# Optimization experiments

Hardware: AMD Instinct MI355X
Metric: run time of the kernel (lower is better)

## Reference

```python
import jax, jax.numpy as jnp
import numpy as np

B, N, DIM, HEADS, DEPTH, MLP = 4, 1024, 256, 4, 4, 1024
DH = DIM // HEADS
EPS = 1e-5


def _ln(x, g, b):
    mu = jnp.mean(x, axis=-1, keepdims=True)
    var = jnp.mean((x - mu) ** 2, axis=-1, keepdims=True)
    return (x - mu) / jnp.sqrt(var + EPS) * g + b


def setup_inputs() -> dict:
    key = jax.random.key(0)
    ks = jax.random.split(key, 10)
    s = 0.02
    p = {}
    p["x"] = jax.random.normal(ks[0], (B, N, DIM), jnp.float32)
    p["attn_bias"] = jax.random.normal(ks[1], (2, B, HEADS, N, N), jnp.float32)
    p["ln1_g"] = jnp.ones((DEPTH, DIM), jnp.float32)
    p["ln1_b"] = jnp.zeros((DEPTH, DIM), jnp.float32)
    p["Wkv"] = jax.random.normal(ks[2], (DEPTH, DIM, 2 * DIM), jnp.float32) * s
    p["Wq"] = jax.random.normal(ks[3], (DEPTH, DIM, DIM), jnp.float32) * s
    p["Wo"] = jax.random.normal(ks[4], (DEPTH, DIM, DIM), jnp.float32) * s
    p["bo"] = jnp.zeros((DEPTH, DIM), jnp.float32)
    p["ln2_g"] = jnp.ones((DEPTH, DIM), jnp.float32)
    p["ln2_b"] = jnp.zeros((DEPTH, DIM), jnp.float32)
    p["W1"] = jax.random.normal(ks[5], (DEPTH, DIM, MLP), jnp.float32) * s
    p["b1"] = jnp.zeros((DEPTH, MLP), jnp.float32)
    p["W2"] = jax.random.normal(ks[6], (DEPTH, MLP, DIM), jnp.float32) * s
    p["b2"] = jnp.zeros((DEPTH, DIM), jnp.float32)
    p["Wg"] = jax.random.normal(ks[7], (DIM, DIM), jnp.float32) * s
    p["lng_g"] = jnp.ones((DIM,), jnp.float32)
    p["lng_b"] = jnp.zeros((DIM,), jnp.float32)
    return p


def reference(x, attn_bias, ln1_g, ln1_b, Wkv, Wq, Wo, bo, ln2_g, ln2_b, W1, b1, W2, b2, Wg, lng_g, lng_b):
    scale = DIM ** -0.5
    add_attn = attn_bias[0] + attn_bias[1]            # [B,H,N,N]
    # aggregation bias matrices are layer-invariant (recomputed identically each layer in torch)
    A = jnp.mean(attn_bias[0], axis=1)                # [B,N,N]
    S = jnp.mean(attn_bias[1], axis=1)
    G = jax.nn.softmax(A * S, axis=2)                 # [B,N,N]

    def split_heads(t):  # [B,N,DIM] -> [B,H,N,DH]
        return t.reshape(B, N, HEADS, DH).transpose(0, 2, 1, 3)

    for l in range(DEPTH):
        # softmax-GCN aggregation
        x_ma = jax.nn.relu(_ln(jnp.matmul(G, x) @ Wg, lng_g, lng_b))
        # attention (PreNorm on x only; q comes from un-normed x_ma)
        xn = _ln(x, ln1_g[l], ln1_b[l])
        kv = xn @ Wkv[l]
        k, v = jnp.split(kv, 2, axis=-1)
        q = x_ma @ Wq[l]
        qh, kh, vh = split_heads(q), split_heads(k), split_heads(v)
        dots = jnp.einsum('bhid,bhjd->bhij', qh, kh) * scale + add_attn
        attn = jax.nn.softmax(dots, axis=-1)
        out = jnp.einsum('bhij,bhjd->bhid', attn, vh)
        out = out.transpose(0, 2, 1, 3).reshape(B, N, DIM)
        x = x + out @ Wo[l] + bo[l]
        # feed-forward (exact GELU, matching torch nn.GELU default)
        xn2 = _ln(x, ln2_g[l], ln2_b[l])
        x = x + jax.nn.gelu(xn2 @ W1[l] + b1[l], approximate=False) @ W2[l] + b2[l]
    return x
```

## Files before the change

### kernel.cpp

```cpp
#include <hip/hip_runtime.h>
#include <hip/hip_bf16.h>
#include <math.h>

typedef unsigned short u16;
typedef __bf16 bf16x8 __attribute__((ext_vector_type(8)));
typedef float f32x4 __attribute__((ext_vector_type(4)));

#define B_ 4
#define N_ 1024
#define DIM_ 256
#define HEADS_ 4
#define DH_ 64
#define MLP_ 1024
#define DEPTH_ 4

__device__ __forceinline__ float r2f(u16 r){ return __uint_as_float(((unsigned)r)<<16); }
__device__ __forceinline__ u16 f2r(float f){ __hip_bfloat16 h = __float2bfloat16(f); return *(u16*)&h; }

__device__ __forceinline__ float gelu_exact(float v){
  return 0.5f*v*(1.0f + erff(v*0.70710678118654752440f));
}

#define MFMA16(a,b,c) __builtin_amdgcn_mfma_f32_16x16x32_bf16(a,b,c,0,0,0)

__global__ void prep_fused(const float* __restrict__ bias, u16* __restrict__ G, u16* __restrict__ bsum,
                           const float* __restrict__ X, u16* __restrict__ Y,
                           const float* __restrict__ g, const float* __restrict__ bvec){
  if (blockIdx.x < 4096){
    int blk = blockIdx.x;
    int i = blk & (N_-1);
    int b = blk >> 10;
    int t = threadIdx.x;
    __shared__ float red[256];
    long long base0 = ((long long)(b*HEADS_)*N_ + i)*(long long)N_;
    const long long hs = (long long)N_*N_;
    const long long cs = (long long)B_*HEADS_*N_*N_;
    int j0 = t*4;
    f32x4 a = {0.f,0.f,0.f,0.f}, s = {0.f,0.f,0.f,0.f};
    #pragma unroll
    for (int h=0;h<HEADS_;h++){
      f32x4 x0 = *(const f32x4*)(bias + base0 + h*hs + j0);
      f32x4 x1 = *(const f32x4*)(bias + cs + base0 + h*hs + j0);
      a += x0; s += x1;
      union { ushort4 u; u16 e[4]; } pk;
      #pragma unroll
      for (int k=0;k<4;k++) pk.e[k] = f2r(x0[k]+x1[k]);
      *(ushort4*)(bsum + base0 + h*hs + j0) = pk.u;
    }
    float v[4]; float lmax = -3e38f;
    #pragma unroll
    for (int k=0;k<4;k++){ v[k] = (a[k]*0.25f)*(s[k]*0.25f); lmax = fmaxf(lmax, v[k]); }
    red[t]=lmax; __syncthreads();
    for (int st=128;st>0;st>>=1){ if(t<st) red[t]=fmaxf(red[t],red[t+st]); __syncthreads(); }
    float m = red[0]; __syncthreads();
    float e[4]; float lsum = 0.f;
    #pragma unroll
    for (int k=0;k<4;k++){ e[k] = __expf(v[k]-m); lsum += e[k]; }
    red[t]=lsum; __syncthreads();
    for (int st=128;st>0;st>>=1){ if(t<st) red[t]+=red[t+st]; __syncthreads(); }
    float inv = 1.0f/red[0];
    u16* Grow = G + ((long long)b*N_ + i)*(long long)N_;
    union { ushort4 u; u16 e[4]; } pg;
    #pragma unroll
    for (int k=0;k<4;k++) pg.e[k] = f2r(e[k]*inv);
    *(ushort4*)(Grow + j0) = pg.u;
  } else {
    int row = (blockIdx.x-4096)*8 + (threadIdx.x>>5);
    int cg = threadIdx.x&31;
    const float* xp = X + (long long)row*DIM_ + cg*8;
    f32x4 v0 = *(const f32x4*)xp;
    f32x4 v1 = *(const f32x4*)(xp+4);
    float s = v0[0]+v0[1]+v0[2]+v0[3]+v1[0]+v1[1]+v1[2]+v1[3];
    s += __shfl_xor(s,1); s += __shfl_xor(s,2); s += __shfl_xor(s,4); s += __shfl_xor(s,8); s += __shfl_xor(s,16);
    float mu = s*(1.0f/256.0f);
    float s2 = 0.f;
    #pragma unroll
    for (int k=0;k<4;k++){ float d=v0[k]-mu; s2 += d*d; }
    #pragma unroll
    for (int k=0;k<4;k++){ float d=v1[k]-mu; s2 += d*d; }
    s2 += __shfl_xor(s2,1); s2 += __shfl_xor(s2,2); s2 += __shfl_xor(s2,4); s2 += __shfl_xor(s2,8); s2 += __shfl_xor(s2,16);
    float rstd = rsqrtf(s2*(1.0f/256.0f)+1e-5f);
    f32x4 g0 = *(const f32x4*)(g + cg*8);
    f32x4 g1 = *(const f32x4*)(g + cg*8 + 4);
    f32x4 b0 = *(const f32x4*)(bvec + cg*8);
    f32x4 b1 = *(const f32x4*)(bvec + cg*8 + 4);
    union { ushort4 u[2]; u16 e[8]; } pk;
    #pragma unroll
    for (int k=0;k<4;k++) pk.e[k]   = f2r((v0[k]-mu)*rstd*g0[k] + b0[k]);
    #pragma unroll
    for (int k=0;k<4;k++) pk.e[4+k] = f2r((v1[k]-mu)*rstd*g1[k] + b1[k]);
    u16* yp = Y + (long long)row*DIM_ + cg*8;
    *(ushort4*)yp = pk.u[0];
    *(ushort4*)(yp+4) = pk.u[1];
  }
}

__global__ void tcast_all(const float* __restrict__ Wkv, const float* __restrict__ Wq,
                          const float* __restrict__ Wo, const float* __restrict__ W1,
                          const float* __restrict__ W2, const float* __restrict__ Wg,
                          const float* __restrict__ xin,
                          u16* WkvT, u16* WqT, u16* WoT, u16* W1T, u16* W2T, u16* WgT, u16* xT){
  int z = blockIdx.z;
  const float* I; u16* O; int ldin, R, C;
  if (z < 4)       { I = Wkv + z*131072;      O = WkvT + z*131072;      ldin=512;  R=256;  C=512;  }
  else if (z < 8)  { I = Wq  + (z-4)*65536;   O = WqT  + (z-4)*65536;   ldin=256;  R=256;  C=256;  }
  else if (z < 12) { I = Wo  + (z-8)*65536;   O = WoT  + (z-8)*65536;   ldin=256;  R=256;  C=256;  }
  else if (z < 16) { I = W1  + (z-12)*262144; O = W1T  + (z-12)*262144; ldin=1024; R=256;  C=1024; }
  else if (z < 20) { I = W2  + (z-16)*262144; O = W2T  + (z-16)*262144; ldin=256;  R=1024; C=256;  }
  else if (z == 20){ I = Wg;                  O = WgT;                  ldin=256;  R=256;  C=256;  }
  else             { I = xin + (z-21)*262144; O = xT   + (z-21)*262144; ldin=256;  R=1024; C=256;  }
  int c0 = blockIdx.x*32, r0 = blockIdx.y*32;
  if (c0 >= C || r0 >= R) return;
  __shared__ float tile[32][33];
  int tx = threadIdx.x, ty = threadIdx.y;
  #pragma unroll
  for (int i=0;i<4;i++)
    tile[ty*4+i][tx] = I[(long long)(r0+ty*4+i)*ldin + c0+tx];
  __syncthreads();
  #pragma unroll
  for (int i=0;i<4;i++)
    O[(long long)(c0+ty*4+i)*R + r0+tx] = f2r(tile[tx][ty*4+i]);
}

__global__ __launch_bounds__(512, 4) void layer_pre(
    const u16* __restrict__ Gb, const u16* __restrict__ xT, const u16* __restrict__ xnb,
    const u16* __restrict__ WgT, const u16* __restrict__ WqT, const u16* __restrict__ WkvT,
    const float* __restrict__ lng, const float* __restrict__ lnb,
    u16* __restrict__ qb, u16* __restrict__ kvb, u16* __restrict__ vt)
{
  __shared__ float Gx_s[16][264];
  __shared__ float t2_s[16][264];
  __shared__ u16  xma_s[16][264];
  int tid = threadIdx.x;
  int w = tid>>6, lane = tid&63, lr = lane&15, qd = lane>>4;
  int bid = blockIdx.x;

  if (bid >= 256){
    int row0 = (bid-256)*16;
    int batch = row0>>10;
    const u16* Ap = xnb + (long long)(row0+lr)*DIM_;
    f32x4 acc[4] = {};
    for (int k0=0;k0<256;k0+=32){
      bf16x8 af = *(const bf16x8*)(Ap + k0 + qd*8);
      #pragma unroll
      for (int i=0;i<4;i++){
        bf16x8 bf = *(const bf16x8*)(WkvT + (long long)((w*4+i)*16+lr)*256 + k0 + qd*8);
        acc[i] = MFMA16(af,bf,acc[i]);
      }
    }
    #pragma unroll
    for (int i=0;i<4;i++){
      int col = (w*4+i)*16+lr;
      #pragma unroll
      for (int r=0;r<4;r++){
        int row = row0+qd*4+r;
        float v = acc[i][r];
        kvb[(long long)row*512 + col] = f2r(v);
        if (col >= 256)
          vt[(long long)batch*262144 + (long long)(col-256)*1024 + (row&1023)] = f2r(v);
      }
    }
    return;
  }

  int row0 = bid*16;
  int batch = row0>>10, brow0 = row0&1023;

  {
    int kw = w>>2, cw = w&3;
    const u16* Ap = Gb + (long long)batch*1048576 + (long long)(brow0+lr)*1024 + kw*512;
    const u16* Bp = xT + (long long)batch*262144 + (long long)kw*512;
    f32x4 acc[4] = {};
    for (int k0=0;k0<512;k0+=32){
      bf16x8 af = *(const bf16x8*)(Ap + k0 + qd*8);
      #pragma unroll
      for (int nt=0;nt<4;nt++){
        bf16x8 bf = *(const bf16x8*)(Bp + (long long)(cw*64+nt*16+lr)*1024 + k0 + qd*8);
        acc[nt] = MFMA16(af,bf,acc[nt]);
      }
    }
    if (kw==0){
      #pragma unroll
      for (int nt=0;nt<4;nt++)
        #pragma unroll
        for (int r=0;r<4;r++) Gx_s[qd*4+r][cw*64+nt*16+lr] = acc[nt][r];
    }
    __syncthreads();
    if (kw==1){
      #pragma unroll
      for (int nt=0;nt<4;nt++)
        #pragma unroll
        for (int r=0;r<4;r++) Gx_s[qd*4+r][cw*64+nt*16+lr] += acc[nt][r];
    }
    __syncthreads();
  }
  {
    int r = tid>>5, cg2 = tid&31;
    #pragma unroll
    for (int i=0;i<8;i++) xma_s[r][cg2*8+i] = f2r(Gx_s[r][cg2*8+i]);
  }
  __syncthreads();
  {
    f32x4 acc[2] = {};
    for (int k0=0;k0<256;k0+=32){
      bf16x8 af = *(const bf16x8*)&xma_s[lr][k0+qd*8];
      #pragma unroll
      for (int i=0;i<2;i++){
        bf16x8 bf = *(const bf16x8*)(WgT + (long long)((w*2+i)*16+lr)*256 + k0 + qd*8);
        acc[i] = MFMA16(af,bf,acc[i]);
      }
    }
    #pragma unroll
    for (int i=0;i<2;i++)
      #pragma unroll
      for (int r=0;r<4;r++) t2_s[qd*4+r][(w*2+i)*16+lr] = acc[i][r];
  }
  __syncthreads();
  {
    int r = tid>>5, cg2 = tid&31;
    float v[8]; float s=0.f;
    #pragma unroll
    for (int i=0;i<8;i++){ v[i] = t2_s[r][cg2*8+i]; s += v[i]; }
    s += __shfl_xor(s,1); s += __shfl_xor(s,2); s += __shfl_xor(s,4); s += __shfl_xor(s,8); s += __shfl_xor(s,16);
    float mu = s*(1.0f/256.0f);
    float s2=0.f;
    #pragma unroll
    for (int i=0;i<8;i++){ float d=v[i]-mu; s2 += d*d; }
    s2 += __shfl_xor(s2,1); s2 += __shfl_xor(s2,2); s2 += __shfl_xor(s2,4); s2 += __shfl_xor(s2,8); s2 += __shfl_xor(s2,16);
    float rstd = rsqrtf(s2*(1.0f/256.0f)+1e-5f);
    #pragma unroll
    for (int i=0;i<8;i++){
      int c = cg2*8+i;
      float y = (v[i]-mu)*rstd*lng[c] + lnb[c];
      xma_s[r][c] = f2r(fmaxf(y,0.f));
    }
  }
  __syncthreads();
  {
    f32x4 acc[2] = {};
    for (int k0=0;k0<256;k0+=32){
      bf16x8 af = *(const bf16x8*)&xma_s[lr][k0+qd*8];
      #pragma unroll
      for (int i=0;i<2;i++){
        bf16x8 bf = *(const bf16x8*)(WqT + (long long)((w*2+i)*16+lr)*256 + k0 + qd*8);
        acc[i] = MFMA16(af,bf,acc[i]);
      }
    }
    #pragma unroll
    for (int i=0;i<2;i++)
      #pragma unroll
      for (int r=0;r<4;r++)
        qb[(long long)(row0+qd*4+r)*DIM_ + (w*2+i)*16+lr] = f2r(acc[i][r]);
  }
}

#define APSMEM 84224
__global__ __launch_bounds__(1024, 4) void attn_post(
    const u16* __restrict__ qb, const u16* __restrict__ kvb,
    const u16* __restrict__ vt, const u16* __restrict__ bsum,
    const float* __restrict__ resx,
    const u16* __restrict__ WoT, const float* __restrict__ bo,
    const float* __restrict__ ln2g, const float* __restrict__ ln2b,
    const u16* __restrict__ W1T, const float* __restrict__ b1,
    const u16* __restrict__ W2T, const float* __restrict__ b2,
    float* __restrict__ xf_out,
    const float* __restrict__ ln1g_next, const float* __restrict__ ln1b_next,
    u16* __restrict__ xn_out, u16* __restrict__ xT_out)
{
  __shared__ __align__(16) char smem[APSMEM];
  u16 (*sb)[16][72]   = (u16 (*)[16][72])smem;
  u16 (*Pl)[16][72]   = (u16 (*)[16][72])(smem+36864);
  float (*Ml)[16]     = (float(*)[16])(smem+73728);
  float (*Ll)[16]     = (float(*)[16])(smem+74752);
  float (*Ol)[16][68] = (float(*)[16][68])smem;
  u16  (*ao_s)[264]   = (u16 (*)[264])(smem+75776);
  float (*v_s)[264]   = (float(*)[264])smem;
  u16  (*xn2_s)[264]  = (u16 (*)[264])(smem+16896);
  u16  (*h1_s)[1048]  = (u16 (*)[1048])(smem+25344);
  float (*xnew_s)[264]= (float(*)[264])(smem+58880);

  int tid = threadIdx.x;
  int w = tid>>6, lane = tid&63, lr = lane&15, qd = lane>>4;
  int row0 = blockIdx.x*16;
  int batch = row0>>10, brow0 = row0&1023;

  f32x4 oacc[4] = {};
  float m_r[4] = {-3e38f,-3e38f,-3e38f,-3e38f};
  float l_r[4] = {0.f,0.f,0.f,0.f};
  {
    int h = w>>2, g = w&3;
    int z = batch*HEADS_ + h;
    const u16* qp = qb + ((long long)row0 + lr)*DIM_ + h*DH_;
    bf16x8 aq0 = *(const bf16x8*)(qp + qd*8);
    bf16x8 aq1 = *(const bf16x8*)(qp + 32 + qd*8);

    const u16* kbase = kvb + ((long long)(batch*N_))*512 + h*DH_;
    const u16* vbase = vt + (long long)batch*(DIM_*N_) + (long long)(h*DH_)*N_;
    const u16* bias_base = bsum + ((long long)z*N_ + brow0)*(long long)N_;
    int srr = lane>>2, scc = (lane&3)*16;

    for (int jtl=0; jtl<4; jtl++){
      int j0 = (g*4 + jtl)*64;
      {
        const u16* gs = bias_base + (long long)srr*N_ + j0 + scc;
        uint4 t0 = *(const uint4*)gs;
        uint4 t1 = *(const uint4*)(gs+8);
        *(uint4*)&sb[w][srr][scc]   = t0;
        *(uint4*)&sb[w][srr][scc+8] = t1;
      }
      f32x4 sacc[4] = {};
      #pragma unroll
      for (int nt=0; nt<4; nt++){
        const u16* kp = kbase + (long long)(j0 + nt*16 + lr)*512;
        bf16x8 bk0 = *(const bf16x8*)(kp + qd*8);
        bf16x8 bk1 = *(const bf16x8*)(kp + 32 + qd*8);
        sacc[nt] = MFMA16(aq0, bk0, sacc[nt]);
        sacc[nt] = MFMA16(aq1, bk1, sacc[nt]);
      }
      #pragma unroll
      for (int r=0;r<4;r++){
        float pv[4];
        float vmax = -3e38f;
        #pragma unroll
        for (int nt=0;nt<4;nt++){
          float v = sacc[nt][r]*0.0625f + r2f(sb[w][qd*4+r][nt*16+lr]);
          pv[nt] = v;
          vmax = fmaxf(vmax, v);
        }
        vmax = fmaxf(vmax, __shfl_xor(vmax,1));
        vmax = fmaxf(vmax, __shfl_xor(vmax,2));
        vmax = fmaxf(vmax, __shfl_xor(vmax,4));
        vmax = fmaxf(vmax, __shfl_xor(vmax,8));
        float newm = fmaxf(m_r[r], vmax);
        float alpha = __expf(m_r[r]-newm);
        m_r[r] = newm;
        float psum = 0.f;
        #pragma unroll
        for (int nt=0;nt<4;nt++){
          float p = __expf(pv[nt]-newm);
          psum += p;
          Pl[w][qd*4+r][nt*16+lr] = f2r(p);
        }
        psum += __shfl_xor(psum,1);
        psum += __shfl_xor(psum,2);
        psum += __shfl_xor(psum,4);
        psum += __shfl_xor(psum,8);
        l_r[r] = l_r[r]*alpha + psum;
        #pragma unroll
        for (int ot=0;ot<4;ot++) oacc[ot][r] *= alpha;
      }
      #pragma unroll
      for (int ks=0;ks<2;ks++){
        bf16x8 ap = *(const bf16x8*)&Pl[w][lr][ks*32 + qd*8];
        #pragma unroll
        for (int ot=0;ot<4;ot++){
          const u16* vp = vbase + (long long)(ot*16+lr)*N_ + j0 + ks*32 + qd*8;
          bf16x8 bv = *(const bf16x8*)vp;
          oacc[ot] = MFMA16(ap, bv, oacc[ot]);
        }
      }
    }
  }
  __syncthreads();
  #pragma unroll
  for (int r=0;r<4;r++){
    int row = qd*4+r;
    #pragma unroll
    for (int ot=0;ot<4;ot++) Ol[w][row][ot*16+lr] = oacc[ot][r];
    if (lr==0){ Ml[w][row] = m_r[r]; Ll[w][row] = l_r[r]; }
  }
  __syncthreads();
  if ((w&3)==0){
    int h = w>>2;
    #pragma unroll
    for (int r=0;r<4;r++){
      int row = qd*4+r;
      float m0 = Ml[w][row], m1 = Ml[w+1][row], m2 = Ml[w+2][row], m3 = Ml[w+3][row];
      float mm = fmaxf(fmaxf(m0,m1), fmaxf(m2,m3));
      float e0 = __expf(m0-mm), e1 = __expf(m1-mm), e2 = __expf(m2-mm), e3 = __expf(m3-mm);
      float inv = 1.0f/(Ll[w][row]*e0 + Ll[w+1][row]*e1 + Ll[w+2][row]*e2 + Ll[w+3][row]*e3);
      #pragma unroll
      for (int ot=0;ot<4;ot++){
        int c = ot*16+lr;
        float o = Ol[w][row][c]*e0 + Ol[w+1][row][c]*e1 + Ol[w+2][row][c]*e2 + Ol[w+3][row][c]*e3;
        ao_s[row][h*DH_ + c] = f2r(o*inv);
      }
    }
  }
  __syncthreads();

  {
    int kw = w>>3, cw = w&7;
    f32x4 acc[2] = {};
    for (int k0=0;k0<128;k0+=32){
      bf16x8 af = *(const bf16x8*)&ao_s[lr][kw*128 + k0 + qd*8];
      #pragma unroll
      for (int i=0;i<2;i++){
        int cv = cw*2+i;
        bf16x8 bf = *(const bf16x8*)(WoT + (long long)(cv*16+lr)*256 + kw*128 + k0 + qd*8);
        acc[i] = MFMA16(af,bf,acc[i]);
      }
    }
    if (kw==0){
      #pragma unroll
      for (int i=0;i<2;i++)
        #pragma unroll
        for (int r=0;r<4;r++) v_s[qd*4+r][(cw*2+i)*16+lr] = acc[i][r];
    }
    __syncthreads();
    if (kw==1){
      #pragma unroll
      for (int i=0;i<2;i++){
        int col = (cw*2+i)*16+lr;
        #pragma unroll
        for (int r=0;r<4;r++)
          v_s[qd*4+r][col] = v_s[qd*4+r][col] + acc[i][r] + bo[col]
                           + resx[(long long)(row0+qd*4+r)*DIM_ + col];
      }
    }
    __syncthreads();
  }
  {
    int r = tid>>6, c0 = (tid&63)*4;
    float v[4]; float s=0.f;
    #pragma unroll
    for (int i=0;i<4;i++){ v[i] = v_s[r][c0+i]; s += v[i]; }
    s += __shfl_xor(s,1); s += __shfl_xor(s,2); s += __shfl_xor(s,4);
    s += __shfl_xor(s,8); s += __shfl_xor(s,16); s += __shfl_xor(s,32);
    float mu = s*(1.0f/256.0f);
    float s2=0.f;
    #pragma unroll
    for (int i=0;i<4;i++){ float d=v[i]-mu; s2 += d*d; }
    s2 += __shfl_xor(s2,1); s2 += __shfl_xor(s2,2); s2 += __shfl_xor(s2,4);
    s2 += __shfl_xor(s2,8); s2 += __shfl_xor(s2,16); s2 += __shfl_xor(s2,32);
    float rstd = rsqrtf(s2*(1.0f/256.0f)+1e-5f);
    #pragma unroll
    for (int i=0;i<4;i++){
      int c = c0+i;
      xn2_s[r][c] = f2r((v[i]-mu)*rstd*ln2g[c] + ln2b[c]);
    }
  }
  __syncthreads();
  {
    f32x4 acc[4] = {};
    for (int k0=0;k0<256;k0+=32){
      bf16x8 af = *(const bf16x8*)&xn2_s[lr][k0+qd*8];
      #pragma unroll
      for (int i=0;i<4;i++){
        int cv = w*4+i;
        bf16x8 bf = *(const bf16x8*)(W1T + (long long)(cv*16+lr)*256 + k0 + qd*8);
        acc[i] = MFMA16(af,bf,acc[i]);
      }
    }
    #pragma unroll
    for (int i=0;i<4;i++){
      int col = (w*4+i)*16+lr;
      #pragma unroll
      for (int r=0;r<4;r++)
        h1_s[qd*4+r][col] = f2r(gelu_exact(acc[i][r] + b1[col]));
    }
  }
  __syncthreads();
  {
    int kw = w>>3, cw = w&7;
    f32x4 acc[2] = {};
    for (int k0=0;k0<512;k0+=32){
      bf16x8 af = *(const bf16x8*)&h1_s[lr][kw*512 + k0 + qd*8];
      #pragma unroll
      for (int i=0;i<2;i++){
        int cv = cw*2+i;
        bf16x8 bf = *(const bf16x8*)(W2T + (long long)(cv*16+lr)*1024 + kw*512 + k0 + qd*8);
        acc[i] = MFMA16(af,bf,acc[i]);
      }
    }
    if (kw==0){
      #pragma unroll
      for (int i=0;i<2;i++)
        #pragma unroll
        for (int r=0;r<4;r++) xnew_s[qd*4+r][(cw*2+i)*16+lr] = acc[i][r];
    }
    __syncthreads();
    if (kw==1){
      #pragma unroll
      for (int i=0;i<2;i++){
        int col = (cw*2+i)*16+lr;
        #pragma unroll
        for (int r=0;r<4;r++){
          float v = xnew_s[qd*4+r][col] + acc[i][r] + b2[col] + v_s[qd*4+r][col];
          xf_out[(long long)(row0+qd*4+r)*DIM_ + col] = v;
          xnew_s[qd*4+r][col] = v;
        }
      }
    }
  }
  if (ln1g_next){
    __syncthreads();
    int r = tid>>6, c0 = (tid&63)*4;
    float v[4]; float s=0.f;
    #pragma unroll
    for (int i=0;i<4;i++){ v[i] = xnew_s[r][c0+i]; s += v[i]; }
    s += __shfl_xor(s,1); s += __shfl_xor(s,2); s += __shfl_xor(s,4);
    s += __shfl_xor(s,8); s += __shfl_xor(s,16); s += __shfl_xor(s,32);
    float mu = s*(1.0f/256.0f);
    float s2=0.f;
    #pragma unroll
    for (int i=0;i<4;i++){ float d=v[i]-mu; s2 += d*d; }
    s2 += __shfl_xor(s2,1); s2 += __shfl_xor(s2,2); s2 += __shfl_xor(s2,4);
    s2 += __shfl_xor(s2,8); s2 += __shfl_xor(s2,16); s2 += __shfl_xor(s2,32);
    float rstd = rsqrtf(s2*(1.0f/256.0f)+1e-5f);
    int grow = row0 + r;
    #pragma unroll
    for (int i=0;i<4;i++){
      int c = c0+i;
      xn_out[(long long)grow*DIM_ + c] = f2r((v[i]-mu)*rstd*ln1g_next[c] + ln1b_next[c]);
      xT_out[(long long)batch*262144 + (long long)c*1024 + (grow&1023)] = f2r(v[i]);
    }
  }
}

extern "C" void kernel_launch(void* const* d_in, const int* in_sizes, int n_in,
                              void* d_out, int out_size, void* d_ws, size_t ws_size,
                              hipStream_t stream){
  const float* x_in   = (const float*)d_in[0];
  const float* abias  = (const float*)d_in[1];
  const float* ln1_g  = (const float*)d_in[2];
  const float* ln1_b  = (const float*)d_in[3];
  const float* Wkv    = (const float*)d_in[4];
  const float* Wq     = (const float*)d_in[5];
  const float* Wo     = (const float*)d_in[6];
  const float* bo     = (const float*)d_in[7];
  const float* ln2_g  = (const float*)d_in[8];
  const float* ln2_b  = (const float*)d_in[9];
  const float* W1     = (const float*)d_in[10];
  const float* b1     = (const float*)d_in[11];
  const float* W2     = (const float*)d_in[12];
  const float* b2     = (const float*)d_in[13];
  const float* Wg     = (const float*)d_in[14];
  const float* lng_g  = (const float*)d_in[15];
  const float* lng_b  = (const float*)d_in[16];

  char* ws = (char*)d_ws;
  float* xf   = (float*)(ws);
  u16*  Gb    = (u16*)(ws + (4ll<<20));
  u16*  bsum  = (u16*)(ws + (12ll<<20));
  u16*  kvb   = (u16*)(ws + (44ll<<20));
  u16*  vt    = (u16*)(ws + (48ll<<20));
  u16*  xT    = (u16*)(ws + (50ll<<20));
  u16*  xnb   = (u16*)(ws + (52ll<<20));
  u16*  qb    = (u16*)(ws + (54ll<<20));
  u16*  WkvT  = (u16*)(ws + (58ll<<20));
  u16*  WqT   = (u16*)(ws + (59ll<<20));
  u16*  WoT   = (u16*)(ws + (59ll<<20) + (512ll<<10));
  u16*  W1T   = (u16*)(ws + (60ll<<20));
  u16*  W2T   = (u16*)(ws + (62ll<<20));
  u16*  WgT   = (u16*)(ws + (64ll<<20));

  prep_fused<<<dim3(4608), dim3(256), 0, stream>>>(abias, Gb, bsum, x_in, xnb, ln1_g, ln1_b);
  tcast_all<<<dim3(32,32,25), dim3(32,8), 0, stream>>>(Wkv,Wq,Wo,W1,W2,Wg,x_in,
                                                       WkvT,WqT,WoT,W1T,W2T,WgT,xT);

  for (int l=0; l<DEPTH_; l++){
    const float* resx = (l==0) ? x_in : xf;
    layer_pre<<<dim3(512), dim3(512), 0, stream>>>(Gb, xT, xnb,
        WgT, WqT + (long long)l*65536, WkvT + (long long)l*131072,
        lng_g, lng_b, qb, kvb, vt);
    if (l < DEPTH_-1){
      attn_post<<<dim3(256), dim3(1024), 0, stream>>>(qb, kvb, vt, bsum, resx,
          WoT + (long long)l*65536, bo + l*DIM_, ln2_g + l*DIM_, ln2_b + l*DIM_,
          W1T + (long long)l*262144, b1 + l*MLP_, W2T + (long long)l*262144, b2 + l*DIM_,
          xf, ln1_g + (l+1)*DIM_, ln1_b + (l+1)*DIM_, xnb, xT);
    } else {
      attn_post<<<dim3(256), dim3(1024), 0, stream>>>(qb, kvb, vt, bsum, resx,
          WoT + (long long)l*65536, bo + l*DIM_, ln2_g + l*DIM_, ln2_b + l*DIM_,
          W1T + (long long)l*262144, b1 + l*MLP_, W2T + (long long)l*262144, b2 + l*DIM_,
          (float*)d_out, nullptr, nullptr, nullptr, nullptr);
    }
  }
}
```

Before: 702.5 us.

## Shrink attn_post LDS via pairwise softmax merge and buffer aliasing

Reuses the bias staging buffer for the P tile, merges the four per-head partial softmax states in a two-step pairwise tree instead of all at once, and aliases the FFN output scratch onto existing buffers. This cuts the kernel's shared memory from about 84 KB to about 59 KB and raises the launch-bounds occupancy hint so more blocks can fit per CU. In exchange it adds extra barriers. The tighter register budget from the higher occupancy hint may also cause spills.

```diff
diff --git a/kernel.cpp b/kernel.cpp
--- a/kernel.cpp
+++ b/kernel.cpp
@@ -254,8 +254,8 @@
   }
 }
 
-#define APSMEM 84224
-__global__ __launch_bounds__(1024, 4) void attn_post(
+#define APSMEM 58880
+__global__ __launch_bounds__(1024, 8) void attn_post(
     const u16* __restrict__ qb, const u16* __restrict__ kvb,
     const u16* __restrict__ vt, const u16* __restrict__ bsum,
     const float* __restrict__ resx,
@@ -269,26 +269,25 @@
 {
   __shared__ __align__(16) char smem[APSMEM];
   u16 (*sb)[16][72]   = (u16 (*)[16][72])smem;
-  u16 (*Pl)[16][72]   = (u16 (*)[16][72])(smem+36864);
-  float (*Ml)[16]     = (float(*)[16])(smem+73728);
-  float (*Ll)[16]     = (float(*)[16])(smem+74752);
-  float (*Ol)[16][68] = (float(*)[16][68])smem;
-  u16  (*ao_s)[264]   = (u16 (*)[264])(smem+75776);
+  float (*Olb)[16][68]= (float(*)[16][68])smem;
+  float (*Mlb)[16]    = (float(*)[16])(smem+34816);
+  float (*Llb)[16]    = (float(*)[16])(smem+35328);
+  u16  (*ao_s)[264]   = (u16 (*)[264])(smem+36864);
   float (*v_s)[264]   = (float(*)[264])smem;
   u16  (*xn2_s)[264]  = (u16 (*)[264])(smem+16896);
   u16  (*h1_s)[1048]  = (u16 (*)[1048])(smem+25344);
-  float (*xnew_s)[264]= (float(*)[264])(smem+58880);
+  float (*p3_s)[264]  = (float(*)[264])(smem+25344);
 
   int tid = threadIdx.x;
   int w = tid>>6, lane = tid&63, lr = lane&15, qd = lane>>4;
   int row0 = blockIdx.x*16;
   int batch = row0>>10, brow0 = row0&1023;
+  int h = w>>2, g = w&3;
 
   f32x4 oacc[4] = {};
   float m_r[4] = {-3e38f,-3e38f,-3e38f,-3e38f};
   float l_r[4] = {0.f,0.f,0.f,0.f};
   {
-    int h = w>>2, g = w&3;
     int z = batch*HEADS_ + h;
     const u16* qp = qb + ((long long)row0 + lr)*DIM_ + h*DH_;
     bf16x8 aq0 = *(const bf16x8*)(qp + qd*8);
@@ -339,7 +338,7 @@
         for (int nt=0;nt<4;nt++){
           float p = __expf(pv[nt]-newm);
           psum += p;
-          Pl[w][qd*4+r][nt*16+lr] = f2r(p);
+          sb[w][qd*4+r][nt*16+lr] = f2r(p);
         }
         psum += __shfl_xor(psum,1);
         psum += __shfl_xor(psum,2);
@@ -351,7 +350,7 @@
       }
       #pragma unroll
       for (int ks=0;ks<2;ks++){
-        bf16x8 ap = *(const bf16x8*)&Pl[w][lr][ks*32 + qd*8];
+        bf16x8 ap = *(const bf16x8*)&sb[w][lr][ks*32 + qd*8];
         #pragma unroll
         for (int ot=0;ot<4;ot++){
           const u16* vp = vbase + (long long)(ot*16+lr)*N_ + j0 + ks*32 + qd*8;
@@ -362,28 +361,55 @@
     }
   }
   __syncthreads();
-  #pragma unroll
-  for (int r=0;r<4;r++){
-    int row = qd*4+r;
-    #pragma unroll
-    for (int ot=0;ot<4;ot++) Ol[w][row][ot*16+lr] = oacc[ot][r];
-    if (lr==0){ Ml[w][row] = m_r[r]; Ll[w][row] = l_r[r]; }
-  }
-  __syncthreads();
-  if ((w&3)==0){
-    int h = w>>2;
+  if (g & 1){
+    int slot = h*2 + (g>>1);
     #pragma unroll
     for (int r=0;r<4;r++){
       int row = qd*4+r;
-      float m0 = Ml[w][row], m1 = Ml[w+1][row], m2 = Ml[w+2][row], m3 = Ml[w+3][row];
-      float mm = fmaxf(fmaxf(m0,m1), fmaxf(m2,m3));
-      float e0 = __expf(m0-mm), e1 = __expf(m1-mm), e2 = __expf(m2-mm), e3 = __expf(m3-mm);
-      float inv = 1.0f/(Ll[w][row]*e0 + Ll[w+1][row]*e1 + Ll[w+2][row]*e2 + Ll[w+3][row]*e3);
+      #pragma unroll
+      for (int ot=0;ot<4;ot++) Olb[slot][row][ot*16+lr] = oacc[ot][r];
+      if (lr==0){ Mlb[slot][row] = m_r[r]; Llb[slot][row] = l_r[r]; }
+    }
+  }
+  __syncthreads();
+  if (!(g & 1)){
+    int slot = h*2 + (g>>1);
+    #pragma unroll
+    for (int r=0;r<4;r++){
+      int row = qd*4+r;
+      float m1 = Mlb[slot][row], l1 = Llb[slot][row];
+      float mm = fmaxf(m_r[r], m1);
+      float e0 = __expf(m_r[r]-mm), e1 = __expf(m1-mm);
+      m_r[r] = mm;
+      l_r[r] = l_r[r]*e0 + l1*e1;
+      #pragma unroll
+      for (int ot=0;ot<4;ot++)
+        oacc[ot][r] = oacc[ot][r]*e0 + Olb[slot][row][ot*16+lr]*e1;
+    }
+  }
+  __syncthreads();
+  if (g == 2){
+    #pragma unroll
+    for (int r=0;r<4;r++){
+      int row = qd*4+r;
+      #pragma unroll
+      for (int ot=0;ot<4;ot++) Olb[h][row][ot*16+lr] = oacc[ot][r];
+      if (lr==0){ Mlb[h][row] = m_r[r]; Llb[h][row] = l_r[r]; }
+    }
+  }
+  __syncthreads();
+  if (g == 0){
+    #pragma unroll
+    for (int r=0;r<4;r++){
+      int row = qd*4+r;
+      float m1 = Mlb[h][row], l1 = Llb[h][row];
+      float mm = fmaxf(m_r[r], m1);
+      float e0 = __expf(m_r[r]-mm), e1 = __expf(m1-mm);
+      float linv = 1.0f/(l_r[r]*e0 + l1*e1);
       #pragma unroll
       for (int ot=0;ot<4;ot++){
-        int c = ot*16+lr;
-        float o = Ol[w][row][c]*e0 + Ol[w+1][row][c]*e1 + Ol[w+2][row][c]*e2 + Ol[w+3][row][c]*e3;
-        ao_s[row][h*DH_ + c] = f2r(o*inv);
+        float o = oacc[ot][r]*e0 + Olb[h][row][ot*16+lr]*e1;
+        ao_s[row][h*DH_ + ot*16+lr] = f2r(o*linv);
       }
     }
   }
@@ -473,11 +499,12 @@
         acc[i] = MFMA16(af,bf,acc[i]);
       }
     }
+    __syncthreads();
     if (kw==0){
       #pragma unroll
       for (int i=0;i<2;i++)
         #pragma unroll
-        for (int r=0;r<4;r++) xnew_s[qd*4+r][(cw*2+i)*16+lr] = acc[i][r];
+        for (int r=0;r<4;r++) p3_s[qd*4+r][(cw*2+i)*16+lr] = acc[i][r];
     }
     __syncthreads();
     if (kw==1){
@@ -486,9 +513,9 @@
         int col = (cw*2+i)*16+lr;
         #pragma unroll
         for (int r=0;r<4;r++){
-          float v = xnew_s[qd*4+r][col] + acc[i][r] + b2[col] + v_s[qd*4+r][col];
+          float v = p3_s[qd*4+r][col] + acc[i][r] + b2[col] + v_s[qd*4+r][col];
           xf_out[(long long)(row0+qd*4+r)*DIM_ + col] = v;
-          xnew_s[qd*4+r][col] = v;
+          v_s[qd*4+r][col] = v;
         }
       }
     }
@@ -498,7 +525,7 @@
     int r = tid>>6, c0 = (tid&63)*4;
     float v[4]; float s=0.f;
     #pragma unroll
-    for (int i=0;i<4;i++){ v[i] = xnew_s[r][c0+i]; s += v[i]; }
+    for (int i=0;i<4;i++){ v[i] = v_s[r][c0+i]; s += v[i]; }
     s += __shfl_xor(s,1); s += __shfl_xor(s,2); s += __shfl_xor(s,4);
     s += __shfl_xor(s,8); s += __shfl_xor(s,16); s += __shfl_xor(s,32);
     float mu = s*(1.0f/256.0f);
```

Result: slower. 753.0 us (+7.2%).
